# Kernel tuning notes

Measured on AMD Instinct MI355X. Metric: run time of the kernel, lower is better.

## Reference

```python
import jax, jax.numpy as jnp
import numpy as np

EPS = 1e-3  # sscp_conv_group_norm_eps


def setup_inputs() -> dict:
    key = jax.random.key(0)
    k1, k2, k3 = jax.random.split(key, 3)
    audio_encodings = jax.random.normal(k1, (4, 1, 4096, 128), dtype=jnp.float32)
    # Conv2d(in=1, out=128, kernel=(3,3), stride=(2,2), bias=False), OIHW layout
    conv_w = jax.random.normal(k2, (128, 1, 3, 3), dtype=jnp.float32) * 0.1
    # AudioCumulativeGroupNorm per-channel scale (init ones; randomize slightly)
    norm_scale = jnp.ones((128,), dtype=jnp.float32) + 0.01 * jax.random.normal(k3, (128,), dtype=jnp.float32)
    return {"audio_encodings": audio_encodings, "conv_w": conv_w, "norm_scale": norm_scale}


def reference(audio_encodings, conv_w, norm_scale):
    # manual_padding = (0, 1, 1, 1) in torch F.pad order (W_left, W_right, H_top, H_bottom)
    x = jnp.pad(audio_encodings, ((0, 0), (0, 0), (1, 1), (0, 1)))
    # Conv2d stride (2,2), no padding, no bias
    y = jax.lax.conv_general_dilated(
        x, conv_w, window_strides=(2, 2), padding='VALID',
        dimension_numbers=('NCHW', 'OIHW', 'NCHW'))  # [B, C, T, F]
    # permute to [B, T, F, C] and normalize cumulatively over T (mask=None)
    h = jnp.transpose(y, (0, 2, 3, 1)).astype(jnp.float32)
    B, T, F, C = h.shape
    # cumulative count of elements per group at each t: (t+1) * F * C
    cnt = (jnp.arange(1, T + 1, dtype=jnp.float32) * (F * C)).reshape(1, T, 1, 1)
    cum_sum = jnp.cumsum(jnp.sum(h, axis=(2, 3), keepdims=True), axis=1)  # [B,T,1,1]
    cum_mean = cum_sum / cnt
    sq = jnp.sum((h - cum_mean) ** 2, axis=(2, 3), keepdims=True)
    cum_var = jnp.cumsum(sq, axis=1) / cnt
    normed = (h - cum_mean) * jax.lax.rsqrt(cum_var + EPS) * norm_scale  # scale per channel (last dim)
    out = jnp.transpose(normed, (0, 3, 1, 2))  # back to [B, C, T, F]
    return jax.nn.relu(out)
```

## Files before the change

kernel.cpp:

```cpp
#include <hip/hip_runtime.h>

#define X_H 4096
#define X_W 128
#define BATCH 4
#define CH 128
#define TT_OUT 2048
#define FF 64
#define EPS_GN 1e-3f

typedef float f4 __attribute__((ext_vector_type(4)));
typedef float f2 __attribute__((ext_vector_type(2)));

#define S1_OFF 0
#define SS_OFF (BATCH*TT_OUT)
#define MI_OFF (2*BATCH*TT_OUT)

__global__ __launch_bounds__(256) void stats_kernel(const float* __restrict__ x,
                                                    const float* __restrict__ w,
                                                    float* __restrict__ ws) {
    __shared__ float Ml[81];
    __shared__ float Wl[9];
    int tid = threadIdx.x;
    if (tid < 81) {
        int j = tid / 9, k = tid % 9;
        float acc = 0.f;
        for (int c = 0; c < CH; ++c) acc = fmaf(w[c*9 + j], w[c*9 + k], acc);
        Ml[tid] = acc;
    } else if (tid < 90) {
        int k = tid - 81;
        float acc = 0.f;
        for (int c = 0; c < CH; ++c) acc += w[c*9 + k];
        Wl[k] = acc;
    }
    __syncthreads();

    int fq = tid & 15;
    int tr = tid >> 4;
    int gt = blockIdx.x * 16 + tr;
    int t = gt & (TT_OUT - 1);
    int b = gt >> 11;
    const float* xb = x + (size_t)b * (X_H * X_W);

    float xr[3][9];
    int r0 = 2*t - 1;
#pragma unroll
    for (int kh = 0; kh < 3; ++kh) {
        int r = r0 + kh;
        if (r >= 0 && r < X_H) {
            const float* rp = xb + (size_t)r * X_W + 8*fq;
            f4 v0 = *(const f4*)rp;
            f4 v1 = *(const f4*)(rp + 4);
            xr[kh][0]=v0.x; xr[kh][1]=v0.y; xr[kh][2]=v0.z; xr[kh][3]=v0.w;
            xr[kh][4]=v1.x; xr[kh][5]=v1.y; xr[kh][6]=v1.z; xr[kh][7]=v1.w;
            xr[kh][8] = (fq == 15) ? 0.f : rp[8];
        } else {
#pragma unroll
            for (int k = 0; k < 9; ++k) xr[kh][k] = 0.f;
        }
    }

    float s1 = 0.f, ss = 0.f;
#pragma unroll
    for (int jf = 0; jf < 4; ++jf) {
        float tv[9];
#pragma unroll
        for (int kh = 0; kh < 3; ++kh)
#pragma unroll
            for (int kw = 0; kw < 3; ++kw)
                tv[kh*3+kw] = xr[kh][2*jf + kw];
#pragma unroll
        for (int k = 0; k < 9; ++k) s1 = fmaf(Wl[k], tv[k], s1);
#pragma unroll
        for (int j = 0; j < 9; ++j) {
            float tj = 0.f;
#pragma unroll
            for (int k = 0; k < 9; ++k) tj = fmaf(Ml[j*9+k], tv[k], tj);
            ss = fmaf(tv[j], tj, ss);
        }
    }
#pragma unroll
    for (int off = 1; off < 16; off <<= 1) {
        s1 += __shfl_xor(s1, off);
        ss += __shfl_xor(ss, off);
    }
    if (fq == 0) {
        ws[S1_OFF + gt] = s1;
        ws[SS_OFF + gt] = ss;
    }
}

__global__ __launch_bounds__(256) void scan_kernel(float* __restrict__ ws) {
    int b = blockIdx.x;
    int tid = threadIdx.x;
    int lane = tid & 63;
    int wv = tid >> 6;
    const float* S1 = ws + S1_OFF + b*TT_OUT;
    const float* SS = ws + SS_OFF + b*TT_OUT;
    f2* MI = (f2*)(ws + MI_OFF) + b*TT_OUT;
    __shared__ double wsum_lds[4];

    double s1loc[8], v[8];
    double tot = 0.0;
#pragma unroll
    for (int i = 0; i < 8; ++i) { s1loc[i] = (double)S1[tid*8+i]; tot += s1loc[i]; v[i] = tot; }
    double incl = tot;
#pragma unroll
    for (int off = 1; off < 64; off <<= 1) {
        double n = __shfl_up(incl, off);
        if (lane >= off) incl += n;
    }
    if (lane == 63) wsum_lds[wv] = incl;
    __syncthreads();
    double woff = 0.0;
    for (int w2 = 0; w2 < wv; ++w2) woff += wsum_lds[w2];
    double prefix = woff + incl - tot;

    double muloc[8], v2[8];
    double tot2 = 0.0;
#pragma unroll
    for (int i = 0; i < 8; ++i) {
        int t = tid*8 + i;
        double cs = prefix + v[i];
        double cnt = (double)(t+1) * 8192.0;
        double mu = cs / cnt;
        double sq = (double)SS[t] - 2.0*mu*s1loc[i] + 8192.0*mu*mu;
        muloc[i] = mu;
        tot2 += sq; v2[i] = tot2;
    }
    double incl2 = tot2;
#pragma unroll
    for (int off = 1; off < 64; off <<= 1) {
        double n = __shfl_up(incl2, off);
        if (lane >= off) incl2 += n;
    }
    __syncthreads();
    if (lane == 63) wsum_lds[wv] = incl2;
    __syncthreads();
    double woff2 = 0.0;
    for (int w2 = 0; w2 < wv; ++w2) woff2 += wsum_lds[w2];
    double prefix2 = woff2 + incl2 - tot2;
#pragma unroll
    for (int i = 0; i < 8; ++i) {
        int t = tid*8 + i;
        double cnt = (double)(t+1) * 8192.0;
        double var = (prefix2 + v2[i]) / cnt;
        f2 mi;
        mi.x = (float)muloc[i];
        mi.y = rsqrtf((float)var + EPS_GN);
        MI[t] = mi;
    }
}

#define T_TILE 16
#define CG 16
__global__ __launch_bounds__(256) void out_kernel(const float* __restrict__ x,
        const float* __restrict__ w, const float* __restrict__ scale,
        const float* __restrict__ ws, float* __restrict__ out) {
    __shared__ float wl[CG][9];
    __shared__ float sl[CG];
    int tid = threadIdx.x;
    int b = blockIdx.z;
    int c0 = blockIdx.y * CG;
    int t0 = blockIdx.x * T_TILE;
    if (tid < CG*9) wl[tid/9][tid%9] = w[c0*9 + tid];
    if (tid < CG) sl[tid] = scale[c0 + tid];
    __syncthreads();

    int fq = tid & 15;
    int tr = tid >> 4;
    int t = t0 + tr;
    const float* xb = x + (size_t)b * (X_H * X_W);
    f2 mi = ((const f2*)(ws + MI_OFF))[b*TT_OUT + t];
    float mu = mi.x, istd = mi.y;

    float xr[3][9];
    int r0 = 2*t - 1;
#pragma unroll
    for (int kh = 0; kh < 3; ++kh) {
        int r = r0 + kh;
        if (r >= 0 && r < X_H) {
            const float* rp = xb + (size_t)r * X_W + 8*fq;
            f4 v0 = *(const f4*)rp;
            f4 v1 = *(const f4*)(rp + 4);
            xr[kh][0]=v0.x; xr[kh][1]=v0.y; xr[kh][2]=v0.z; xr[kh][3]=v0.w;
            xr[kh][4]=v1.x; xr[kh][5]=v1.y; xr[kh][6]=v1.z; xr[kh][7]=v1.w;
            xr[kh][8] = (fq == 15) ? 0.f : rp[8];
        } else {
#pragma unroll
            for (int k = 0; k < 9; ++k) xr[kh][k] = 0.f;
        }
    }

    float* ob = out + (((size_t)(b*CH + c0) * TT_OUT + t) * FF + 4*fq);
#pragma unroll
    for (int c = 0; c < CG; ++c) {
        float a  = istd * sl[c];
        float nb = -mu * a;
        f4 v;
#pragma unroll
        for (int jf = 0; jf < 4; ++jf) {
            float h = 0.f;
#pragma unroll
            for (int kh = 0; kh < 3; ++kh)
#pragma unroll
                for (int kw = 0; kw < 3; ++kw)
                    h = fmaf(wl[c][kh*3+kw], xr[kh][2*jf + kw], h);
            float val = fmaxf(fmaf(h, a, nb), 0.f);
            v[jf] = val;
        }
        __builtin_nontemporal_store(v, (f4*)(ob + (size_t)c * (TT_OUT * FF)));
    }
}

extern "C" void kernel_launch(void* const* d_in, const int* in_sizes, int n_in,
                              void* d_out, int out_size, void* d_ws, size_t ws_size,
                              hipStream_t stream) {
    const float* x     = (const float*)d_in[0];
    const float* w     = (const float*)d_in[1];
    const float* scale = (const float*)d_in[2];
    float* out = (float*)d_out;
    float* ws  = (float*)d_ws;

    stats_kernel<<<(BATCH*TT_OUT)/16, 256, 0, stream>>>(x, w, ws);
    scan_kernel<<<BATCH, 256, 0, stream>>>(ws);
    out_kernel<<<dim3(TT_OUT/T_TILE, CH/CG, BATCH), 256, 0, stream>>>(x, w, scale, ws, out);
}
```

Before: 62.66 us.

## Use fp32 scan, stage weights in LDS, widen channel group in output kernel

Result: slower. 65.60 us (+4.7%).

```diff
diff --git a/kernel.cpp b/kernel.cpp
--- a/kernel.cpp
+++ b/kernel.cpp
@@ -18,18 +18,24 @@
 __global__ __launch_bounds__(256) void stats_kernel(const float* __restrict__ x,
                                                     const float* __restrict__ w,
                                                     float* __restrict__ ws) {
+    __shared__ float wlds[CH*9];
     __shared__ float Ml[81];
     __shared__ float Wl[9];
     int tid = threadIdx.x;
+#pragma unroll
+    for (int i = tid; i < CH*9; i += 256) wlds[i] = w[i];
+    __syncthreads();
     if (tid < 81) {
         int j = tid / 9, k = tid % 9;
         float acc = 0.f;
-        for (int c = 0; c < CH; ++c) acc = fmaf(w[c*9 + j], w[c*9 + k], acc);
+#pragma unroll 8
+        for (int c = 0; c < CH; ++c) acc = fmaf(wlds[c*9 + j], wlds[c*9 + k], acc);
         Ml[tid] = acc;
     } else if (tid < 90) {
         int k = tid - 81;
         float acc = 0.f;
-        for (int c = 0; c < CH; ++c) acc += w[c*9 + k];
+#pragma unroll 8
+        for (int c = 0; c < CH; ++c) acc += wlds[c*9 + k];
         Wl[k] = acc;
     }
     __syncthreads();
@@ -94,65 +100,70 @@
     int tid = threadIdx.x;
     int lane = tid & 63;
     int wv = tid >> 6;
-    const float* S1 = ws + S1_OFF + b*TT_OUT;
-    const float* SS = ws + SS_OFF + b*TT_OUT;
+    const f4* S1v = (const f4*)(ws + S1_OFF + b*TT_OUT);
+    const f4* SSv = (const f4*)(ws + SS_OFF + b*TT_OUT);
     f2* MI = (f2*)(ws + MI_OFF) + b*TT_OUT;
-    __shared__ double wsum_lds[4];
-
-    double s1loc[8], v[8];
-    double tot = 0.0;
-#pragma unroll
-    for (int i = 0; i < 8; ++i) { s1loc[i] = (double)S1[tid*8+i]; tot += s1loc[i]; v[i] = tot; }
-    double incl = tot;
+    __shared__ float wsum_lds[4];
+
+    f4 a0 = S1v[tid*2], a1 = S1v[tid*2+1];
+    f4 b0 = SSv[tid*2], b1 = SSv[tid*2+1];
+    float s1loc[8] = {a0.x,a0.y,a0.z,a0.w,a1.x,a1.y,a1.z,a1.w};
+    float ssloc[8] = {b0.x,b0.y,b0.z,b0.w,b1.x,b1.y,b1.z,b1.w};
+
+    float v[8];
+    float tot = 0.f;
+#pragma unroll
+    for (int i = 0; i < 8; ++i) { tot += s1loc[i]; v[i] = tot; }
+    float incl = tot;
 #pragma unroll
     for (int off = 1; off < 64; off <<= 1) {
-        double n = __shfl_up(incl, off);
+        float n = __shfl_up(incl, off);
         if (lane >= off) incl += n;
     }
     if (lane == 63) wsum_lds[wv] = incl;
     __syncthreads();
-    double woff = 0.0;
+    float woff = 0.f;
     for (int w2 = 0; w2 < wv; ++w2) woff += wsum_lds[w2];
-    double prefix = woff + incl - tot;
-
-    double muloc[8], v2[8];
-    double tot2 = 0.0;
+    float prefix = woff + incl - tot;
+
+    float muloc[8], v2[8];
+    float tot2 = 0.f;
 #pragma unroll
     for (int i = 0; i < 8; ++i) {
         int t = tid*8 + i;
-        double cs = prefix + v[i];
-        double cnt = (double)(t+1) * 8192.0;
-        double mu = cs / cnt;
-        double sq = (double)SS[t] - 2.0*mu*s1loc[i] + 8192.0*mu*mu;
+        float cs = prefix + v[i];
+        float cnt = (float)(t+1) * 8192.f;
+        float mu = cs / cnt;
+        float sq = ssloc[i] - 2.f*mu*s1loc[i] + 8192.f*mu*mu;
         muloc[i] = mu;
         tot2 += sq; v2[i] = tot2;
     }
-    double incl2 = tot2;
+    float incl2 = tot2;
 #pragma unroll
     for (int off = 1; off < 64; off <<= 1) {
-        double n = __shfl_up(incl2, off);
+        float n = __shfl_up(incl2, off);
         if (lane >= off) incl2 += n;
     }
     __syncthreads();
     if (lane == 63) wsum_lds[wv] = incl2;
     __syncthreads();
-    double woff2 = 0.0;
+    float woff2 = 0.f;
     for (int w2 = 0; w2 < wv; ++w2) woff2 += wsum_lds[w2];
-    double prefix2 = woff2 + incl2 - tot2;
+    float prefix2 = woff2 + incl2 - tot2;
 #pragma unroll
     for (int i = 0; i < 8; ++i) {
         int t = tid*8 + i;
-        double cnt = (double)(t+1) * 8192.0;
-        double var = (prefix2 + v2[i]) / cnt;
+        float cnt = (float)(t+1) * 8192.f;
+        float var = (prefix2 + v2[i]) / cnt;
         f2 mi;
-        mi.x = (float)muloc[i];
-        mi.y = rsqrtf((float)var + EPS_GN);
+        mi.x = muloc[i];
+        mi.y = rsqrtf(var + EPS_GN);
         MI[t] = mi;
     }
 }
 
 #define T_TILE 16
-#define CG 16
+#define CG 32
 __global__ __launch_bounds__(256) void out_kernel(const float* __restrict__ x,
         const float* __restrict__ w, const float* __restrict__ scale,
         const float* __restrict__ ws, float* __restrict__ out) {
@@ -162,7 +173,7 @@
     int b = blockIdx.z;
     int c0 = blockIdx.y * CG;
     int t0 = blockIdx.x * T_TILE;
-    if (tid < CG*9) wl[tid/9][tid%9] = w[c0*9 + tid];
+    for (int i = tid; i < CG*9; i += 256) wl[i/9][i%9] = w[c0*9 + i];
     if (tid < CG) sl[tid] = scale[c0 + tid];
     __syncthreads();
 
@@ -205,8 +216,7 @@
 #pragma unroll
                 for (int kw = 0; kw < 3; ++kw)
                     h = fmaf(wl[c][kh*3+kw], xr[kh][2*jf + kw], h);
-            float val = fmaxf(fmaf(h, a, nb), 0.f);
-            v[jf] = val;
+            v[jf] = fmaxf(fmaf(h, a, nb), 0.f);
         }
         __builtin_nontemporal_store(v, (f4*)(ob + (size_t)c * (TT_OUT * FF)));
     }
```
